# Performance work log

Measured on AMD Instinct MI355X. Metric: run time of the kernel, lower is better.

The kernel has to match this reference:

```python
import jax, jax.numpy as jnp
import numpy as np

B, C, H, W = 4, 128, 96, 96
E = 4
C8 = C // 8


def _conv1x1(w, b, x):
    # w: [out, in], x: [b, in, H, W]
    return jnp.einsum('oi,bihw->bohw', w, x) + b[None, :, None, None]


def _bilinear_zeros(x, gx, gy):
    # x: [b, C, h, w]; gx, gy: [b, H2, W2] normalized coords in [-1, 1]
    # align_corners=True, padding_mode='zeros' (matches F.grid_sample)
    b, c, h, w = x.shape
    ix = (gx + 1.0) * 0.5 * (w - 1)
    iy = (gy + 1.0) * 0.5 * (h - 1)
    ix0 = jnp.floor(ix)
    iy0 = jnp.floor(iy)
    tx = ix - ix0
    ty = iy - iy0
    ix0 = ix0.astype(jnp.int32)
    iy0 = iy0.astype(jnp.int32)

    def gather(yy, xx):
        valid = ((xx >= 0) & (xx < w) & (yy >= 0) & (yy < h)).astype(x.dtype)
        xc = jnp.clip(xx, 0, w - 1)
        yc = jnp.clip(yy, 0, h - 1)
        vals = jax.vmap(lambda xb, y, xi: xb[:, y, xi])(x, yc, xc)  # [b,C,H2,W2]
        return vals * valid[:, None]

    w00 = ((1 - tx) * (1 - ty))[:, None]
    w01 = (tx * (1 - ty))[:, None]
    w10 = ((1 - tx) * ty)[:, None]
    w11 = (tx * ty)[:, None]
    return (gather(iy0, ix0) * w00 + gather(iy0, ix0 + 1) * w01
            + gather(iy0 + 1, ix0) * w10 + gather(iy0 + 1, ix0 + 1) * w11)


def setup_inputs() -> dict:
    key = jax.random.key(0)
    ks = jax.random.split(key, 12)
    s = 0.05
    return {
        'x': jax.random.normal(ks[0], (B, C, H, W), jnp.float32),
        'weight_compress': jax.random.normal(ks[1], (E, C8, C), jnp.float32) * s,
        'weight_expand': jax.random.normal(ks[2], (E, C, C8), jnp.float32) * s,
        'body_w1': jax.random.normal(ks[3], (64, 3), jnp.float32) * s,
        'body_b1': jax.random.normal(ks[4], (64,), jnp.float32) * s,
        'body_w2': jax.random.normal(ks[5], (64, 64), jnp.float32) * s,
        'body_b2': jax.random.normal(ks[6], (64,), jnp.float32) * s,
        'rout_w': jax.random.normal(ks[7], (E, 64), jnp.float32) * s,
        'rout_b': jax.random.normal(ks[8], (E,), jnp.float32) * s,
        'off_w': jax.random.normal(ks[9], (2, 64), jnp.float32) * s,
        'off_b': jax.random.normal(ks[10], (2,), jnp.float32) * s,
        'scale': 2,
    }


def reference(x, weight_compress, weight_expand, body_w1, body_b1,
              body_w2, body_b2, rout_w, rout_b, off_w, off_b, scale):
    b, c, h, w = x.shape
    sc = float(scale)
    H2 = round(h * sc)
    W2 = round(w * sc)

    # fractional sub-pixel coordinates (meta-upsample positional encoding)
    ch = (jnp.arange(H2, dtype=jnp.float32) + 0.5) / sc
    ch = ch - jnp.floor(ch + 0.001) - 0.5  # [H2]
    cw = (jnp.arange(W2, dtype=jnp.float32) + 0.5) / sc
    cw = cw - jnp.floor(cw + 0.001) - 0.5  # [W2]
    inp = jnp.stack([
        jnp.full((H2, W2), 1.0 / sc, jnp.float32),
        jnp.broadcast_to(ch[:, None], (H2, W2)),
        jnp.broadcast_to(cw[None, :], (H2, W2)),
    ], axis=0)[None]  # [1, 3, H2, W2]

    emb = jax.nn.relu(_conv1x1(body_w1, body_b1, inp))
    emb = jax.nn.relu(_conv1x1(body_w2, body_b2, emb))
    offset = _conv1x1(off_w, off_b, emb)                      # [1, 2, H2, W2]
    routing = jax.nn.sigmoid(_conv1x1(rout_w, rout_b, emb))   # [1, E, H2, W2]
    r = routing[0].transpose(1, 2, 0)                         # [H2, W2, E]

    # base sampling grid, align_corners=True normalization + learned offset
    gx = ((jnp.arange(W2, dtype=jnp.float32) + 0.5) / sc - 0.5) * 2.0 / (w - 1) - 1.0
    gy = ((jnp.arange(H2, dtype=jnp.float32) + 0.5) / sc - 0.5) * 2.0 / (h - 1) - 1.0
    gx = gx[None, None, :] + offset[:, 0] * 2.0 / (w - 1)     # [1, H2, W2]
    gy = gy[None, :, None] + offset[:, 1] * 2.0 / (h - 1)
    gx = jnp.broadcast_to(gx, (b, H2, W2))
    gy = jnp.broadcast_to(gy, (b, H2, W2))

    fea0 = _bilinear_zeros(x, gx, gy)          # [b, C, H2, W2]
    fea = fea0.transpose(0, 2, 3, 1)           # [b, H2, W2, C]

    # per-pixel routed 1x1 convs: compress (C->C/8) then expand (C/8->C)
    comp = jnp.einsum('bhwc,hwe,eoc->bhwo', fea, r, weight_compress)
    out = jnp.einsum('bhwo,hwe,eco->bhwc', comp, r, weight_expand)
    return out.transpose(0, 3, 1, 2) + fea0
```

## Files before the change

kernel.cpp:

```cpp
#include <hip/hip_runtime.h>
#include <math.h>

#define Bn 4
#define Cc 128
#define Hh 96
#define Ww 96
#define H2c 192
#define W2c 192
#define HW (Hh*Ww)

#define WC_OFF 0
#define WE_OFF (4*2048)
#define TAP_OFF (8*2048)

__global__ __launch_bounds__(256) void k1_mix(
    const float* __restrict__ wcomp, const float* __restrict__ wexp,
    const float* __restrict__ bw1, const float* __restrict__ bb1,
    const float* __restrict__ bw2, const float* __restrict__ bb2,
    const float* __restrict__ rw,  const float* __restrict__ rb,
    const float* __restrict__ ow,  const float* __restrict__ ob,
    float* __restrict__ ws)
{
    __shared__ float e1[64], e2[64], rr[4], of[2];
    const int tid   = threadIdx.x;
    const int cls   = blockIdx.x >> 4;
    const int chunk = blockIdx.x & 15;
    const float chv = (cls & 2) ? 0.25f : -0.25f;
    const float cwv = (cls & 1) ? 0.25f : -0.25f;

    if (tid < 64) {
        float h = bw1[tid*3+0]*0.5f + bw1[tid*3+1]*chv + bw1[tid*3+2]*cwv + bb1[tid];
        e1[tid] = fmaxf(h, 0.f);
    }
    __syncthreads();
    if (tid < 64) {
        float s = bb2[tid];
        for (int i = 0; i < 64; ++i) s += bw2[tid*64+i]*e1[i];
        e2[tid] = fmaxf(s, 0.f);
    }
    __syncthreads();
    if (tid < 6) {
        if (tid < 4) {
            float s = rb[tid];
            for (int i = 0; i < 64; ++i) s += rw[tid*64+i]*e2[i];
            rr[tid] = 1.f/(1.f+expf(-s));
        } else {
            const int d = tid - 4;
            float s = ob[d];
            for (int i = 0; i < 64; ++i) s += ow[d*64+i]*e2[i];
            of[d] = s;
        }
    }
    __syncthreads();
    const float r0 = rr[0], r1 = rr[1], r2 = rr[2], r3 = rr[3];

    if (tid < 128) {
        const int idx = chunk*128 + tid;
        const int o = idx >> 7, c = idx & 127;
        const float v = r0*wcomp[idx] + r1*wcomp[2048+idx]
                      + r2*wcomp[4096+idx] + r3*wcomp[6144+idx];
        ws[WC_OFF + cls*2048 + c*16 + o] = v;
    } else {
        const int idx = chunk*128 + (tid - 128);
        ws[WE_OFF + cls*2048 + idx] =
            r0*wexp[idx] + r1*wexp[2048+idx] + r2*wexp[4096+idx] + r3*wexp[6144+idx];
    }
    if (chunk == 0 && tid == 0) {
        const float fx = cwv + of[0];
        const float fy = chv + of[1];
        const float Dx = floorf(fx), Dy = floorf(fy);
        ws[TAP_OFF + cls*4 + 0] = fx - Dx;
        ws[TAP_OFF + cls*4 + 1] = fy - Dy;
        ws[TAP_OFF + cls*4 + 2] = Dx;
        ws[TAP_OFF + cls*4 + 3] = Dy;
    }
}

__device__ __forceinline__ void remap_axis(int c0, int last, float w0, float w1,
                                           int& base, float& a0, float& a1)
{
    base = min(max(c0, 0), last - 1);
    if (c0 >= 0 && c0 < last) { a0 = w0;  a1 = w1;  }
    else if (c0 == -1)        { a0 = w1;  a1 = 0.f; }
    else if (c0 == last)      { a0 = 0.f; a1 = w0;  }
    else                      { a0 = 0.f; a1 = 0.f; }
}

__global__ __launch_bounds__(256) void k2_fused(
    const float* __restrict__ x, const float* __restrict__ wsr,
    float* __restrict__ out)
{
    __shared__ __align__(16) float lWc[2048];
    __shared__ __align__(16) float lWe[2048];
    __shared__ float lPart[4*16*64];

    const int tid = threadIdx.x;
    const int xl  = tid & 63;
    const int grp = tid >> 6;

    const int n = blockIdx.x;
    const int w = (n & 7) * 288 + (n >> 3);
    const int px = w & 1, py = (w >> 1) & 1;
    const int w2 = w >> 2;
    const int tile = w2 % 144;
    const int b    = w2 / 144;
    const int cls  = (py << 1) | px;

    {
        const float4* sc = reinterpret_cast<const float4*>(wsr + WC_OFF + cls*2048);
        const float4* se = reinterpret_cast<const float4*>(wsr + WE_OFF + cls*2048);
        float4* dc = reinterpret_cast<float4*>(lWc);
        float4* de = reinterpret_cast<float4*>(lWe);
        dc[tid] = sc[tid]; dc[tid+256] = sc[tid+256];
        de[tid] = se[tid]; de[tid+256] = se[tid+256];
    }

    const int idx = tile*64 + xl;
    const int j = idx / 96;
    const int i = idx - j*96;

    const float tx = wsr[TAP_OFF + cls*4 + 0];
    const float ty = wsr[TAP_OFF + cls*4 + 1];
    const int   Dx = (int)wsr[TAP_OFF + cls*4 + 2];
    const int   Dy = (int)wsr[TAP_OFF + cls*4 + 3];
    int cb, rbw; float ax0, ax1, ay0, ay1;
    remap_axis(i + Dx, Ww - 1, 1.f - tx, tx, cb,  ax0, ax1);
    remap_axis(j + Dy, Hh - 1, 1.f - ty, ty, rbw, ay0, ay1);
    const float w00 = ay0*ax0, w01 = ay0*ax1, w10 = ay1*ax0, w11 = ay1*ax1;
    const float* xb = x + (size_t)b*Cc*HW + rbw*Ww + cb;
    __syncthreads();

    float comp[16];
    #pragma unroll
    for (int o = 0; o < 16; ++o) comp[o] = 0.f;
    float fea[32];

    #pragma unroll
    for (int kk = 0; kk < 32; ++kk) {
        const int c = grp*32 + kk;
        const float* p = xb + (size_t)c*HW;
        const float f = w00*p[0] + w01*p[1] + w10*p[Ww] + w11*p[Ww+1];
        fea[kk] = f;
        const float4* wq = reinterpret_cast<const float4*>(lWc + c*16);
        const float4 q0 = wq[0], q1 = wq[1], q2 = wq[2], q3 = wq[3];
        comp[ 0] += q0.x*f; comp[ 1] += q0.y*f; comp[ 2] += q0.z*f; comp[ 3] += q0.w*f;
        comp[ 4] += q1.x*f; comp[ 5] += q1.y*f; comp[ 6] += q1.z*f; comp[ 7] += q1.w*f;
        comp[ 8] += q2.x*f; comp[ 9] += q2.y*f; comp[10] += q2.z*f; comp[11] += q2.w*f;
        comp[12] += q3.x*f; comp[13] += q3.y*f; comp[14] += q3.z*f; comp[15] += q3.w*f;
    }
    #pragma unroll
    for (int o = 0; o < 16; ++o) lPart[(grp*16 + o)*64 + xl] = comp[o];
    __syncthreads();

    #pragma unroll
    for (int jj = 0; jj < 4; ++jj) {
        const int o = grp*4 + jj;
        const float s = lPart[(o     )*64 + xl] + lPart[(16 + o)*64 + xl]
                      + lPart[(32 + o)*64 + xl] + lPart[(48 + o)*64 + xl];
        lPart[o*64 + xl] = s;
    }
    __syncthreads();

    float cf[16];
    #pragma unroll
    for (int o = 0; o < 16; ++o) cf[o] = lPart[o*64 + xl];

    const int xg = 2*i + px;
    const int yg = 2*j + py;
    float* op = out + ((size_t)(b*Cc)*H2c + yg)*W2c + xg;

    #pragma unroll
    for (int kk = 0; kk < 32; ++kk) {
        const int c = grp*32 + kk;
        const float4* wq = reinterpret_cast<const float4*>(lWe + c*16);
        const float4 q0 = wq[0], q1 = wq[1], q2 = wq[2], q3 = wq[3];
        float acc = fea[kk]
            + q0.x*cf[ 0] + q0.y*cf[ 1] + q0.z*cf[ 2] + q0.w*cf[ 3]
            + q1.x*cf[ 4] + q1.y*cf[ 5] + q1.z*cf[ 6] + q1.w*cf[ 7]
            + q2.x*cf[ 8] + q2.y*cf[ 9] + q2.z*cf[10] + q2.w*cf[11]
            + q3.x*cf[12] + q3.y*cf[13] + q3.z*cf[14] + q3.w*cf[15];
        op[(size_t)c*(H2c*W2c)] = acc;
    }
}

extern "C" void kernel_launch(void* const* d_in, const int* in_sizes, int n_in,
                              void* d_out, int out_size, void* d_ws, size_t ws_size,
                              hipStream_t stream) {
    const float* x     = (const float*)d_in[0];
    const float* wcomp = (const float*)d_in[1];
    const float* wexp  = (const float*)d_in[2];
    const float* bw1   = (const float*)d_in[3];
    const float* bb1   = (const float*)d_in[4];
    const float* bw2   = (const float*)d_in[5];
    const float* bb2   = (const float*)d_in[6];
    const float* rw    = (const float*)d_in[7];
    const float* rb    = (const float*)d_in[8];
    const float* ow    = (const float*)d_in[9];
    const float* ob    = (const float*)d_in[10];
    float* out = (float*)d_out;
    float* ws  = (float*)d_ws;

    k1_mix<<<64, 256, 0, stream>>>(wcomp, wexp, bw1, bb1, bw2, bb2, rw, rb, ow, ob, ws);
    k2_fused<<<2304, 256, 0, stream>>>(x, ws, out);
}
```

Before: 43.19 us.

## Process two adjacent source pixels per thread with shared 4-wide tap loads

Each thread now handles two horizontally adjacent low-res pixels of the same class, loading a 2x4 window of x with float2 loads and folding bilinear weights into per-pixel 4-tap coefficient vectors. This halves the grid, reuses the weight LDS reads across two pixels, and cuts per-pixel load instructions. Launch bounds request 3 blocks per CU. In exchange register pressure roughly doubles (fea and comp arrays), and output stores become stride-2 with gaps, which may hurt write coalescing.

```diff
diff --git a/kernel.cpp b/kernel.cpp
--- a/kernel.cpp
+++ b/kernel.cpp
@@ -86,100 +86,152 @@
     else                      { a0 = 0.f; a1 = 0.f; }
 }
 
-__global__ __launch_bounds__(256) void k2_fused(
+__global__ __launch_bounds__(256, 3) void k2_fused(
     const float* __restrict__ x, const float* __restrict__ wsr,
     float* __restrict__ out)
 {
     __shared__ __align__(16) float lWc[2048];
     __shared__ __align__(16) float lWe[2048];
-    __shared__ float lPart[4*16*64];
+    __shared__ __align__(16) float lPart[4*16*128];
 
     const int tid = threadIdx.x;
     const int xl  = tid & 63;
     const int grp = tid >> 6;
 
     const int n = blockIdx.x;
-    const int w = (n & 7) * 288 + (n >> 3);
-    const int px = w & 1, py = (w >> 1) & 1;
-    const int w2 = w >> 2;
-    const int tile = w2 % 144;
-    const int b    = w2 / 144;
-    const int cls  = (py << 1) | px;
+    const int w = (n & 7) * 144 + (n >> 3);
+    const int cls  = w & 3;
+    const int px   = cls & 1, py = (cls >> 1) & 1;
+    const int rest = w >> 2;
+    const int tile = rest % 72;
+    const int b    = rest / 72;
 
     {
         const float4* sc = reinterpret_cast<const float4*>(wsr + WC_OFF + cls*2048);
         const float4* se = reinterpret_cast<const float4*>(wsr + WE_OFF + cls*2048);
-        float4* dc = reinterpret_cast<float4*>(lWc);
-        float4* de = reinterpret_cast<float4*>(lWe);
-        dc[tid] = sc[tid]; dc[tid+256] = sc[tid+256];
-        de[tid] = se[tid]; de[tid+256] = se[tid+256];
-    }
-
-    const int idx = tile*64 + xl;
-    const int j = idx / 96;
-    const int i = idx - j*96;
+        reinterpret_cast<float4*>(lWc)[tid]     = sc[tid];
+        reinterpret_cast<float4*>(lWc)[tid+256] = sc[tid+256];
+        reinterpret_cast<float4*>(lWe)[tid]     = se[tid];
+        reinterpret_cast<float4*>(lWe)[tid+256] = se[tid+256];
+    }
+
+    const int pix0 = (tile*64 + xl)*2;
+    const int j  = pix0 / 96;
+    const int i0 = pix0 - j*96;
 
     const float tx = wsr[TAP_OFF + cls*4 + 0];
     const float ty = wsr[TAP_OFF + cls*4 + 1];
     const int   Dx = (int)wsr[TAP_OFF + cls*4 + 2];
     const int   Dy = (int)wsr[TAP_OFF + cls*4 + 3];
-    int cb, rbw; float ax0, ax1, ay0, ay1;
-    remap_axis(i + Dx, Ww - 1, 1.f - tx, tx, cb,  ax0, ax1);
+
+    int rbw; float ay0, ay1;
     remap_axis(j + Dy, Hh - 1, 1.f - ty, ty, rbw, ay0, ay1);
-    const float w00 = ay0*ax0, w01 = ay0*ax1, w10 = ay1*ax0, w11 = ay1*ax1;
-    const float* xb = x + (size_t)b*Cc*HW + rbw*Ww + cb;
-    __syncthreads();
-
-    float comp[16];
-    #pragma unroll
-    for (int o = 0; o < 16; ++o) comp[o] = 0.f;
-    float fea[32];
+
+    int base = i0 + Dx;
+    base = max(0, min(Ww - 4, base));
+    base &= ~1;
+
+    float bt[2][4], bb_[2][4];
+    #pragma unroll
+    for (int p = 0; p < 2; ++p) {
+        int bp; float a0, a1;
+        remap_axis(i0 + p + Dx, Ww - 1, 1.f - tx, tx, bp, a0, a1);
+        const int k = bp - base;
+        const float c0 = (k == 0) ? a0 : 0.f;
+        const float c1 = (k == 0) ? a1 : ((k == 1) ? a0 : 0.f);
+        const float c2 = (k == 1) ? a1 : ((k == 2) ? a0 : 0.f);
+        const float c3 = (k == 2) ? a1 : 0.f;
+        bt[p][0]  = ay0*c0; bt[p][1]  = ay0*c1; bt[p][2]  = ay0*c2; bt[p][3]  = ay0*c3;
+        bb_[p][0] = ay1*c0; bb_[p][1] = ay1*c1; bb_[p][2] = ay1*c2; bb_[p][3] = ay1*c3;
+    }
+
+    const float* xb = x + (size_t)b*Cc*HW + rbw*Ww + base;
+    __syncthreads();
+
+    float fea[2][32];
+    float comp[2][16];
+    #pragma unroll
+    for (int o = 0; o < 16; ++o) { comp[0][o] = 0.f; comp[1][o] = 0.f; }
 
     #pragma unroll
     for (int kk = 0; kk < 32; ++kk) {
         const int c = grp*32 + kk;
         const float* p = xb + (size_t)c*HW;
-        const float f = w00*p[0] + w01*p[1] + w10*p[Ww] + w11*p[Ww+1];
-        fea[kk] = f;
-        const float4* wq = reinterpret_cast<const float4*>(lWc + c*16);
-        const float4 q0 = wq[0], q1 = wq[1], q2 = wq[2], q3 = wq[3];
-        comp[ 0] += q0.x*f; comp[ 1] += q0.y*f; comp[ 2] += q0.z*f; comp[ 3] += q0.w*f;
-        comp[ 4] += q1.x*f; comp[ 5] += q1.y*f; comp[ 6] += q1.z*f; comp[ 7] += q1.w*f;
-        comp[ 8] += q2.x*f; comp[ 9] += q2.y*f; comp[10] += q2.z*f; comp[11] += q2.w*f;
-        comp[12] += q3.x*f; comp[13] += q3.y*f; comp[14] += q3.z*f; comp[15] += q3.w*f;
-    }
-    #pragma unroll
-    for (int o = 0; o < 16; ++o) lPart[(grp*16 + o)*64 + xl] = comp[o];
+        const float2 t0 = *reinterpret_cast<const float2*>(p);
+        const float2 t1 = *reinterpret_cast<const float2*>(p + 2);
+        const float2 u0 = *reinterpret_cast<const float2*>(p + Ww);
+        const float2 u1 = *reinterpret_cast<const float2*>(p + Ww + 2);
+        const float f0 = bt[0][0]*t0.x + bt[0][1]*t0.y + bt[0][2]*t1.x + bt[0][3]*t1.y
+                       + bb_[0][0]*u0.x + bb_[0][1]*u0.y + bb_[0][2]*u1.x + bb_[0][3]*u1.y;
+        const float f1 = bt[1][0]*t0.x + bt[1][1]*t0.y + bt[1][2]*t1.x + bt[1][3]*t1.y
+                       + bb_[1][0]*u0.x + bb_[1][1]*u0.y + bb_[1][2]*u1.x + bb_[1][3]*u1.y;
+        fea[0][kk] = f0;
+        fea[1][kk] = f1;
+        const float4 q0 = *reinterpret_cast<const float4*>(lWc + c*16 +  0);
+        const float4 q1 = *reinterpret_cast<const float4*>(lWc + c*16 +  4);
+        const float4 q2 = *reinterpret_cast<const float4*>(lWc + c*16 +  8);
+        const float4 q3 = *reinterpret_cast<const float4*>(lWc + c*16 + 12);
+        comp[0][ 0] += q0.x*f0; comp[0][ 1] += q0.y*f0; comp[0][ 2] += q0.z*f0; comp[0][ 3] += q0.w*f0;
+        comp[0][ 4] += q1.x*f0; comp[0][ 5] += q1.y*f0; comp[0][ 6] += q1.z*f0; comp[0][ 7] += q1.w*f0;
+        comp[0][ 8] += q2.x*f0; comp[0][ 9] += q2.y*f0; comp[0][10] += q2.z*f0; comp[0][11] += q2.w*f0;
+        comp[0][12] += q3.x*f0; comp[0][13] += q3.y*f0; comp[0][14] += q3.z*f0; comp[0][15] += q3.w*f0;
+        comp[1][ 0] += q0.x*f1; comp[1][ 1] += q0.y*f1; comp[1][ 2] += q0.z*f1; comp[1][ 3] += q0.w*f1;
+        comp[1][ 4] += q1.x*f1; comp[1][ 5] += q1.y*f1; comp[1][ 6] += q1.z*f1; comp[1][ 7] += q1.w*f1;
+        comp[1][ 8] += q2.x*f1; comp[1][ 9] += q2.y*f1; comp[1][10] += q2.z*f1; comp[1][11] += q2.w*f1;
+        comp[1][12] += q3.x*f1; comp[1][13] += q3.y*f1; comp[1][14] += q3.z*f1; comp[1][15] += q3.w*f1;
+    }
+    #pragma unroll
+    for (int o = 0; o < 16; ++o) {
+        const float2 v = {comp[0][o], comp[1][o]};
+        *reinterpret_cast<float2*>(&lPart[(grp*16 + o)*128 + 2*xl]) = v;
+    }
     __syncthreads();
 
     #pragma unroll
     for (int jj = 0; jj < 4; ++jj) {
         const int o = grp*4 + jj;
-        const float s = lPart[(o     )*64 + xl] + lPart[(16 + o)*64 + xl]
-                      + lPart[(32 + o)*64 + xl] + lPart[(48 + o)*64 + xl];
-        lPart[o*64 + xl] = s;
-    }
-    __syncthreads();
-
-    float cf[16];
-    #pragma unroll
-    for (int o = 0; o < 16; ++o) cf[o] = lPart[o*64 + xl];
-
-    const int xg = 2*i + px;
+        float sx = 0.f, sy = 0.f;
+        #pragma unroll
+        for (int g = 0; g < 4; ++g) {
+            const float2 v = *reinterpret_cast<const float2*>(&lPart[(g*16 + o)*128 + 2*xl]);
+            sx += v.x; sy += v.y;
+        }
+        const float2 s = {sx, sy};
+        *reinterpret_cast<float2*>(&lPart[o*128 + 2*xl]) = s;
+    }
+    __syncthreads();
+
+    float cf[2][16];
+    #pragma unroll
+    for (int o = 0; o < 16; ++o) {
+        const float2 v = *reinterpret_cast<const float2*>(&lPart[o*128 + 2*xl]);
+        cf[0][o] = v.x; cf[1][o] = v.y;
+    }
+
     const int yg = 2*j + py;
+    const int xg = 2*i0 + px;
     float* op = out + ((size_t)(b*Cc)*H2c + yg)*W2c + xg;
 
     #pragma unroll
     for (int kk = 0; kk < 32; ++kk) {
         const int c = grp*32 + kk;
-        const float4* wq = reinterpret_cast<const float4*>(lWe + c*16);
-        const float4 q0 = wq[0], q1 = wq[1], q2 = wq[2], q3 = wq[3];
-        float acc = fea[kk]
-            + q0.x*cf[ 0] + q0.y*cf[ 1] + q0.z*cf[ 2] + q0.w*cf[ 3]
-            + q1.x*cf[ 4] + q1.y*cf[ 5] + q1.z*cf[ 6] + q1.w*cf[ 7]
-            + q2.x*cf[ 8] + q2.y*cf[ 9] + q2.z*cf[10] + q2.w*cf[11]
-            + q3.x*cf[12] + q3.y*cf[13] + q3.z*cf[14] + q3.w*cf[15];
-        op[(size_t)c*(H2c*W2c)] = acc;
+        const float4 q0 = *reinterpret_cast<const float4*>(lWe + c*16 +  0);
+        const float4 q1 = *reinterpret_cast<const float4*>(lWe + c*16 +  4);
+        const float4 q2 = *reinterpret_cast<const float4*>(lWe + c*16 +  8);
+        const float4 q3 = *reinterpret_cast<const float4*>(lWe + c*16 + 12);
+        const float a0 = fea[0][kk]
+            + q0.x*cf[0][ 0] + q0.y*cf[0][ 1] + q0.z*cf[0][ 2] + q0.w*cf[0][ 3]
+            + q1.x*cf[0][ 4] + q1.y*cf[0][ 5] + q1.z*cf[0][ 6] + q1.w*cf[0][ 7]
+            + q2.x*cf[0][ 8] + q2.y*cf[0][ 9] + q2.z*cf[0][10] + q2.w*cf[0][11]
+            + q3.x*cf[0][12] + q3.y*cf[0][13] + q3.z*cf[0][14] + q3.w*cf[0][15];
+        const float a1 = fea[1][kk]
+            + q0.x*cf[1][ 0] + q0.y*cf[1][ 1] + q0.z*cf[1][ 2] + q0.w*cf[1][ 3]
+            + q1.x*cf[1][ 4] + q1.y*cf[1][ 5] + q1.z*cf[1][ 6] + q1.w*cf[1][ 7]
+            + q2.x*cf[1][ 8] + q2.y*cf[1][ 9] + q2.z*cf[1][10] + q2.w*cf[1][11]
+            + q3.x*cf[1][12] + q3.y*cf[1][13] + q3.z*cf[1][14] + q3.w*cf[1][15];
+        float* dst = op + (size_t)c*(H2c*W2c);
+        dst[0] = a0;
+        dst[2] = a1;
     }
 }
 
@@ -201,5 +253,5 @@
     float* ws  = (float*)d_ws;
 
     k1_mix<<<64, 256, 0, stream>>>(wcomp, wexp, bw1, bb1, bw2, bb2, rw, rb, ow, ob, ws);
-    k2_fused<<<2304, 256, 0, stream>>>(x, ws, out);
-}
+    k2_fused<<<1152, 256, 0, stream>>>(x, ws, out);
+}
```

After: 63.24 us. 1.46x slower.
